# Performance work log

Hardware: AMD Instinct MI355X
Metric: run time of the kernel (lower is better)

The kernel has to match this reference:

```python
import jax, jax.numpy as jnp
import numpy as np

B, N, IN_DIM, HIDDEN, OUT_DIM, HEADS = 4, 2048, 64, 128, 128, 4
NEG_INF = -1e9
EPS = 1e-12  # matches tf.math.l2_normalize epsilon


def setup_inputs() -> dict:
    key = jax.random.key(0)
    ks = jax.random.split(key, 13)
    d1 = HIDDEN // HEADS
    d2 = OUT_DIM // HEADS
    s = lambda k, shape, fan: jax.random.normal(k, shape, jnp.float32) * (1.0 / np.sqrt(fan))
    return {
        "x": jax.random.normal(ks[0], (B, N, IN_DIM), jnp.float32),
        "embedding": s(ks[1], (N, HIDDEN), HIDDEN),
        "Wp": s(ks[2], (IN_DIM, HIDDEN), IN_DIM),
        "bp": jnp.zeros((HIDDEN,), jnp.float32),
        "W1": s(ks[3], (HIDDEN, HIDDEN), HIDDEN),
        "a1_src": s(ks[4], (HEADS, d1), d1),
        "a1_dst": s(ks[5], (HEADS, d1), d1),
        "b1": jnp.zeros((HIDDEN,), jnp.float32),
        "W2": s(ks[6], (HIDDEN, OUT_DIM), HIDDEN),
        "a2_src": s(ks[7], (HEADS, d2), d2),
        "a2_dst": s(ks[8], (HEADS, d2), d2),
        "b2": jnp.zeros((OUT_DIM,), jnp.float32),
    }


def _gat(h, mask, W, a_src, a_dst, b, heads):
    # h: [B,N,F_in], mask: [N,N] bool (adj > 0.5), W: [F_in, heads*d]
    Bn, Nn, _ = h.shape
    d = W.shape[1] // heads
    hh = (h @ W).reshape(Bn, Nn, heads, d)                 # [B,N,H,D]
    s_src = jnp.einsum('bnhd,hd->bnh', hh, a_src)          # score of source node j
    s_dst = jnp.einsum('bnhd,hd->bnh', hh, a_dst)          # score of target node i
    # e[b,i,j,h]: raw attention logit for edge j -> i
    e = jax.nn.leaky_relu(s_dst[:, :, None, :] + s_src[:, None, :, :], 0.2)
    e = jnp.where(mask[None, :, :, None], e, NEG_INF)
    alpha = jax.nn.softmax(e, axis=2)                      # softmax over neighbors j
    out = jnp.einsum('bijh,bjhd->bihd', alpha, hh)         # aggregate messages
    return out.reshape(Bn, Nn, heads * d) + b


def reference(x, embedding, Wp, bp, W1, a1_src, a1_dst, b1, W2, a2_src, a2_dst, b2):
    # AdaptiveAdjacency: cosine similarity of learned node embeddings
    ne = embedding * jax.lax.rsqrt(jnp.sum(embedding * embedding, -1, keepdims=True) + EPS)
    adj = ne @ ne.T                                        # [N,N]
    mask = adj > 0.5                                       # dynamic edge set (diag always True)
    h = x @ Wp + bp                                        # Dense projection
    h = jax.nn.gelu(_gat(h, mask, W1, a1_src, a1_dst, b1, HEADS), approximate=False)
    return _gat(h, mask, W2, a2_src, a2_dst, b2, HEADS)
```

## Files before the change

kernel.cpp:

```cpp
#include <hip/hip_runtime.h>
#include <hip/hip_bf16.h>

using u64 = unsigned long long;

constexpr int Bb    = 4;
constexpr int Nn    = 2048;
constexpr int INDIM = 64;
constexpr int HID   = 128;
constexpr int NW    = Nn / 64;
constexpr int NT    = 16;
constexpr int NTRI  = NT * (NT + 1) / 2;

struct AdjS {
    float As[32][132];
    float Bs[32][132];
    float nA[128];
    float nB[128];
    unsigned char mb [128][16];
    unsigned char mbT[128][16];
};

__global__ __launch_bounds__(256) void k_adjproj(
        const float* __restrict__ emb, u64* __restrict__ maskw,
        const float* __restrict__ x,   const float* __restrict__ Wp,
        const float* __restrict__ bp,  const float* __restrict__ W1,
        const float* __restrict__ a1s, const float* __restrict__ a1d,
        float* __restrict__ hh1, float* __restrict__ s1s, float* __restrict__ s1d) {
    __shared__ __align__(16) unsigned char smem[sizeof(AdjS)];
    const int t = threadIdx.x;

    if (blockIdx.x < NTRI) {
        AdjS& S = *reinterpret_cast<AdjS*>(smem);
        int b = blockIdx.x, ti = 0, cum = 0;
        while (cum + (NT - ti) <= b) { cum += NT - ti; ++ti; }
        const int tj = ti + (b - cum);
        const bool diag = (ti == tj);
        const int i0 = ti * 128, j0 = tj * 128;

        const int tx = t & 15, ty = t >> 4;
        const int sr = t >> 1, sh = (t & 1) * 16;

        float acc[8][8];
        #pragma unroll
        for (int a = 0; a < 8; ++a)
            #pragma unroll
            for (int c = 0; c < 8; ++c) acc[a][c] = 0.f;

        float sqa = 0.f, sqb = 0.f;

        for (int kc = 0; kc < HID; kc += 32) {
            const float* gA = emb + (size_t)(i0 + sr) * HID + kc + sh;
            const float* gB = emb + (size_t)(j0 + sr) * HID + kc + sh;
            #pragma unroll
            for (int e = 0; e < 16; e += 4) {
                const float4 va = *reinterpret_cast<const float4*>(gA + e);
                const float4 vb = *reinterpret_cast<const float4*>(gB + e);
                S.As[sh + e + 0][sr] = va.x; S.As[sh + e + 1][sr] = va.y;
                S.As[sh + e + 2][sr] = va.z; S.As[sh + e + 3][sr] = va.w;
                sqa += va.x * va.x + va.y * va.y + va.z * va.z + va.w * va.w;
                S.Bs[sh + e + 0][sr] = vb.x; S.Bs[sh + e + 1][sr] = vb.y;
                S.Bs[sh + e + 2][sr] = vb.z; S.Bs[sh + e + 3][sr] = vb.w;
                sqb += vb.x * vb.x + vb.y * vb.y + vb.z * vb.z + vb.w * vb.w;
            }
            __syncthreads();
            #pragma unroll 4
            for (int k = 0; k < 32; ++k) {
                float a[8], c[8];
                *reinterpret_cast<float4*>(&a[0]) = *reinterpret_cast<const float4*>(&S.As[k][ty * 8]);
                *reinterpret_cast<float4*>(&a[4]) = *reinterpret_cast<const float4*>(&S.As[k][ty * 8 + 4]);
                *reinterpret_cast<float4*>(&c[0]) = *reinterpret_cast<const float4*>(&S.Bs[k][tx * 8]);
                *reinterpret_cast<float4*>(&c[4]) = *reinterpret_cast<const float4*>(&S.Bs[k][tx * 8 + 4]);
                #pragma unroll
                for (int ii = 0; ii < 8; ++ii)
                    #pragma unroll
                    for (int jj = 0; jj < 8; ++jj)
                        acc[ii][jj] += a[ii] * c[jj];
            }
            __syncthreads();
        }

        {
            const float ta = sqa + __shfl_xor(sqa, 1, 64);
            if ((t & 1) == 0) S.nA[sr] = rsqrtf(ta + 1e-12f);
            const float tb = sqb + __shfl_xor(sqb, 1, 64);
            if ((t & 1) == 0) S.nB[sr] = rsqrtf(tb + 1e-12f);
        }
        __syncthreads();

        float rsi[8], rsj[8];
        #pragma unroll
        for (int e = 0; e < 8; ++e) { rsi[e] = S.nA[ty * 8 + e]; rsj[e] = S.nB[tx * 8 + e]; }

        bool bit[8][8];
        #pragma unroll
        for (int e = 0; e < 8; ++e)
            #pragma unroll
            for (int jj = 0; jj < 8; ++jj)
                bit[e][jj] = (acc[e][jj] * rsi[e] * rsj[jj] > 0.5f);

        #pragma unroll
        for (int e = 0; e < 8; ++e) {
            unsigned byte = 0;
            #pragma unroll
            for (int jj = 0; jj < 8; ++jj) if (bit[e][jj]) byte |= (1u << jj);
            S.mb[ty * 8 + e][tx] = (unsigned char)byte;
        }
        #pragma unroll
        for (int jj = 0; jj < 8; ++jj) {
            unsigned byte = 0;
            #pragma unroll
            for (int e = 0; e < 8; ++e) if (bit[e][jj]) byte |= (1u << e);
            S.mbT[tx * 8 + jj][ty] = (unsigned char)byte;
        }
        __syncthreads();

        if (t < 128) {
            const u64* p = reinterpret_cast<const u64*>(S.mb[t]);
            maskw[(size_t)(i0 + t) * NW + 2 * tj]     = p[0];
            maskw[(size_t)(i0 + t) * NW + 2 * tj + 1] = p[1];
        } else if (!diag) {
            const int c = t - 128;
            const u64* p = reinterpret_cast<const u64*>(S.mbT[c]);
            maskw[(size_t)(j0 + c) * NW + 2 * ti]     = p[0];
            maskw[(size_t)(j0 + c) * NW + 2 * ti + 1] = p[1];
        }
    } else {
        float (*hl)[128] = reinterpret_cast<float(*)[128]>(smem);
        const int h  = t >> 7;
        const int c  = t & 127;
        const int r0 = (blockIdx.x - NTRI) * 16 + h * 8;

        float acc[8];
        const float bias = bp[c];
        #pragma unroll
        for (int r = 0; r < 8; ++r) acc[r] = bias;
        #pragma unroll 4
        for (int k = 0; k < INDIM; ++k) {
            const float wp = Wp[k * HID + c];
            #pragma unroll
            for (int r = 0; r < 8; ++r)
                acc[r] += x[(size_t)(r0 + r) * INDIM + k] * wp;
        }
        #pragma unroll
        for (int r = 0; r < 8; ++r) hl[h * 8 + r][c] = acc[r];
        __syncthreads();

        float a2[8];
        #pragma unroll
        for (int r = 0; r < 8; ++r) a2[r] = 0.f;
        #pragma unroll 4
        for (int k = 0; k < HID; ++k) {
            const float w = W1[k * HID + c];
            #pragma unroll
            for (int r = 0; r < 8; ++r)
                a2[r] += hl[h * 8 + r][k] * w;
        }
        const float as = a1s[c], ad = a1d[c];
        #pragma unroll
        for (int r = 0; r < 8; ++r) {
            hh1[(size_t)(r0 + r) * HID + c] = a2[r];
            float vs = a2[r] * as;
            float vd = a2[r] * ad;
            #pragma unroll
            for (int m = 1; m < 32; m <<= 1) {
                vs += __shfl_xor(vs, m, 32);
                vd += __shfl_xor(vd, m, 32);
            }
            if ((c & 31) == 0) {
                s1s[(size_t)(r0 + r) * 4 + (c >> 5)] = vs;
                s1d[(size_t)(r0 + r) * 4 + (c >> 5)] = vd;
            }
        }
    }
}

__global__ __launch_bounds__(128) void k_layer2(
        const float* __restrict__ hh1,
        const float* __restrict__ s1s, const float* __restrict__ s1d,
        const u64* __restrict__ maskw, const float* __restrict__ b1v,
        const float* __restrict__ W2,
        const float* __restrict__ a2s, const float* __restrict__ a2d,
        const float* __restrict__ b2v, float* __restrict__ out) {
    const int r0    = blockIdx.x * 8;
    const int bb    = r0 >> 11;
    const int iBase = r0 & (Nn - 1);
    const int t     = threadIdx.x;
    const int wv    = t >> 6;
    const int lane  = t & 63;
    const int h0    = lane >> 5, h1 = 2 + h0;
    __shared__ float gl[8][128];
    __shared__ float h2l[8][128];
    __shared__ float s2sl[8][4];
    __shared__ float s2dl[8][4];

    for (int rr = 0; rr < 4; ++rr) {
        const int r   = wv * 4 + rr;
        const int row = r0 + r, i = row & (Nn - 1);
        const u64* mrow = maskw + (size_t)i * NW;
        const u64 myw = (lane < NW) ? mrow[lane] : 0ULL;
        u64 nz = __ballot(myw != 0ULL);
        const float sd0 = s1d[(size_t)row * 4 + h0];
        const float sd1 = s1d[(size_t)row * 4 + h1];
        float m0 = -INFINITY, l0 = 0.f, a0 = 0.f;
        float m1 = -INFINITY, l1 = 0.f, a1 = 0.f;
        while (nz) {
            const int w = __builtin_ctzll(nz); nz &= nz - 1;
            u64 word = __shfl(myw, w, 64);
            while (word) {
                const int bit = __builtin_ctzll(word); word &= word - 1;
                const int jr = (bb << 11) + (w << 6) + bit;
                float e0 = sd0 + s1s[(size_t)jr * 4 + h0];
                e0 = e0 > 0.f ? e0 : 0.2f * e0;
                float e1 = sd1 + s1s[(size_t)jr * 4 + h1];
                e1 = e1 > 0.f ? e1 : 0.2f * e1;
                const float v0 = hh1[(size_t)jr * HID + lane];
                const float v1 = hh1[(size_t)jr * HID + 64 + lane];
                float nm = fmaxf(m0, e0);
                float sc = __expf(m0 - nm);
                float p  = __expf(e0 - nm);
                l0 = l0 * sc + p; a0 = a0 * sc + p * v0; m0 = nm;
                nm = fmaxf(m1, e1);
                sc = __expf(m1 - nm);
                p  = __expf(e1 - nm);
                l1 = l1 * sc + p; a1 = a1 * sc + p * v1; m1 = nm;
            }
        }
        float o0 = (l0 > 0.f ? a0 / l0 : 0.f) + b1v[lane];
        float o1 = (l1 > 0.f ? a1 / l1 : 0.f) + b1v[64 + lane];
        o0 = 0.5f * o0 * (1.f + erff(o0 * 0.70710678118654752f));
        o1 = 0.5f * o1 * (1.f + erff(o1 * 0.70710678118654752f));
        gl[r][lane]      = o0;
        gl[r][64 + lane] = o1;
    }
    __syncthreads();

    {
        const int c = t;
        float acc[8];
        #pragma unroll
        for (int r = 0; r < 8; ++r) acc[r] = 0.f;
        #pragma unroll 4
        for (int k = 0; k < HID; ++k) {
            const float w = W2[k * HID + c];
            #pragma unroll
            for (int r = 0; r < 8; ++r)
                acc[r] += gl[r][k] * w;
        }
        const float as = a2s[c], ad = a2d[c];
        #pragma unroll
        for (int r = 0; r < 8; ++r) {
            h2l[r][c] = acc[r];
            float vs = acc[r] * as;
            float vd = acc[r] * ad;
            #pragma unroll
            for (int m = 1; m < 32; m <<= 1) {
                vs += __shfl_xor(vs, m, 32);
                vd += __shfl_xor(vd, m, 32);
            }
            if ((c & 31) == 0) {
                s2sl[r][c >> 5] = vs;
                s2dl[r][c >> 5] = vd;
            }
        }
    }
    __syncthreads();

    for (int rr = 0; rr < 4; ++rr) {
        const int r   = wv * 4 + rr;
        const int row = r0 + r, i = row & (Nn - 1);
        const u64* mrow = maskw + (size_t)i * NW;
        const u64 myw = (lane < NW) ? mrow[lane] : 0ULL;
        u64 nz = __ballot(myw != 0ULL);
        const float sd0 = s2dl[r][h0];
        const float sd1 = s2dl[r][h1];
        float m0 = -INFINITY, l0 = 0.f, a0 = 0.f;
        float m1 = -INFINITY, l1 = 0.f, a1 = 0.f;
        while (nz) {
            const int w = __builtin_ctzll(nz); nz &= nz - 1;
            u64 word = __shfl(myw, w, 64);
            while (word) {
                const int bit = __builtin_ctzll(word); word &= word - 1;
                const int j = (w << 6) + bit;
                float vs0, vs1, v0, v1;
                const unsigned lj = (unsigned)(j - iBase);
                if (lj < 8u) {
                    vs0 = s2sl[lj][h0]; vs1 = s2sl[lj][h1];
                    v0  = h2l[lj][lane]; v1 = h2l[lj][64 + lane];
                } else {
                    const int jr = (bb << 11) + j;
                    const u64* mrj = maskw + (size_t)j * NW;
                    const u64 myj = (lane < NW) ? mrj[lane] : 0ULL;
                    u64 nzj = __ballot(myj != 0ULL);
                    const float sdj0 = s1d[(size_t)jr * 4 + h0];
                    const float sdj1 = s1d[(size_t)jr * 4 + h1];
                    float fm0 = -INFINITY, fl0 = 0.f, fa0 = 0.f;
                    float fm1 = -INFINITY, fl1 = 0.f, fa1 = 0.f;
                    while (nzj) {
                        const int w2 = __builtin_ctzll(nzj); nzj &= nzj - 1;
                        u64 wd = __shfl(myj, w2, 64);
                        while (wd) {
                            const int b2i = __builtin_ctzll(wd); wd &= wd - 1;
                            const int k2 = (bb << 11) + (w2 << 6) + b2i;
                            float e0 = sdj0 + s1s[(size_t)k2 * 4 + h0];
                            e0 = e0 > 0.f ? e0 : 0.2f * e0;
                            float e1 = sdj1 + s1s[(size_t)k2 * 4 + h1];
                            e1 = e1 > 0.f ? e1 : 0.2f * e1;
                            const float fv0 = hh1[(size_t)k2 * HID + lane];
                            const float fv1 = hh1[(size_t)k2 * HID + 64 + lane];
                            float nm = fmaxf(fm0, e0);
                            float sc = __expf(fm0 - nm);
                            float p  = __expf(e0 - nm);
                            fl0 = fl0 * sc + p; fa0 = fa0 * sc + p * fv0; fm0 = nm;
                            nm = fmaxf(fm1, e1);
                            sc = __expf(fm1 - nm);
                            p  = __expf(e1 - nm);
                            fl1 = fl1 * sc + p; fa1 = fa1 * sc + p * fv1; fm1 = nm;
                        }
                    }
                    float g0 = (fl0 > 0.f ? fa0 / fl0 : 0.f) + b1v[lane];
                    float g1 = (fl1 > 0.f ? fa1 / fl1 : 0.f) + b1v[64 + lane];
                    g0 = 0.5f * g0 * (1.f + erff(g0 * 0.70710678118654752f));
                    g1 = 0.5f * g1 * (1.f + erff(g1 * 0.70710678118654752f));
                    float val0 = 0.f, val1 = 0.f;
                    for (int k = 0; k < 64; ++k) {
                        const float gk = __shfl(g0, k, 64);
                        val0 += gk * W2[k * HID + lane];
                        val1 += gk * W2[k * HID + 64 + lane];
                    }
                    for (int k = 0; k < 64; ++k) {
                        const float gk = __shfl(g1, k, 64);
                        val0 += gk * W2[(64 + k) * HID + lane];
                        val1 += gk * W2[(64 + k) * HID + 64 + lane];
                    }
                    float t0 = val0 * a2s[lane];
                    float t1 = val1 * a2s[64 + lane];
                    #pragma unroll
                    for (int m = 1; m < 32; m <<= 1) {
                        t0 += __shfl_xor(t0, m, 32);
                        t1 += __shfl_xor(t1, m, 32);
                    }
                    vs0 = t0; vs1 = t1; v0 = val0; v1 = val1;
                }
                float e0 = sd0 + vs0;
                e0 = e0 > 0.f ? e0 : 0.2f * e0;
                float e1 = sd1 + vs1;
                e1 = e1 > 0.f ? e1 : 0.2f * e1;
                float nm = fmaxf(m0, e0);
                float sc = __expf(m0 - nm);
                float p  = __expf(e0 - nm);
                l0 = l0 * sc + p; a0 = a0 * sc + p * v0; m0 = nm;
                nm = fmaxf(m1, e1);
                sc = __expf(m1 - nm);
                p  = __expf(e1 - nm);
                l1 = l1 * sc + p; a1 = a1 * sc + p * v1; m1 = nm;
            }
        }
        out[(size_t)row * HID + lane]      = (l0 > 0.f ? a0 / l0 : 0.f) + b2v[lane];
        out[(size_t)row * HID + 64 + lane] = (l1 > 0.f ? a1 / l1 : 0.f) + b2v[64 + lane];
    }
}

extern "C" void kernel_launch(void* const* d_in, const int* in_sizes, int n_in,
                              void* d_out, int out_size, void* d_ws, size_t ws_size,
                              hipStream_t stream) {
    const float* x   = (const float*)d_in[0];
    const float* emb = (const float*)d_in[1];
    const float* Wp  = (const float*)d_in[2];
    const float* bp  = (const float*)d_in[3];
    const float* W1  = (const float*)d_in[4];
    const float* a1s = (const float*)d_in[5];
    const float* a1d = (const float*)d_in[6];
    const float* b1  = (const float*)d_in[7];
    const float* W2  = (const float*)d_in[8];
    const float* a2s = (const float*)d_in[9];
    const float* a2d = (const float*)d_in[10];
    const float* b2  = (const float*)d_in[11];

    char* ws = (char*)d_ws;
    u64*  maskw = (u64*)ws;   ws += (size_t)Nn * NW * 8;
    float* hh1  = (float*)ws; ws += (size_t)Bb * Nn * HID * 4;
    float* s1s  = (float*)ws; ws += (size_t)Bb * Nn * 4 * 4;
    float* s1d  = (float*)ws; ws += (size_t)Bb * Nn * 4 * 4;

    k_adjproj<<<NTRI + 512, 256, 0, stream>>>(emb, maskw, x, Wp, bp, W1, a1s, a1d,
                                              hh1, s1s, s1d);
    k_layer2<<<Bb * Nn / 8, 128, 0, stream>>>(hh1, s1s, s1d, maskw, b1,
                                              W2, a2s, a2d, b2, (float*)d_out);
}
```

Baseline: 47.54 us.

## Split adjacency tiles into column halves and widen layer-2 blocks to 16 rows

Each 128x128 triangular adjacency tile is now computed by two blocks, each covering 64 columns. This doubles the number of adjacency blocks so the heavy GEMM-style phase spreads across more compute units. The mask words are packed from 4-bit nibbles, and transposed writes are restricted to 64 columns. The layer-2 kernel now processes 16 rows per block with 256 threads, so more neighbours fall inside the locally cached rows and fewer need the expensive recomputation path. The cost is fewer layer-2 blocks and more redundant A-tile loads for the adjacency phase.

```diff
diff --git a/kernel.cpp b/kernel.cpp
--- a/kernel.cpp
+++ b/kernel.cpp
@@ -10,14 +10,15 @@
 constexpr int NW    = Nn / 64;
 constexpr int NT    = 16;
 constexpr int NTRI  = NT * (NT + 1) / 2;
+constexpr int NADJ  = NTRI * 2;
 
 struct AdjS {
     float As[32][132];
-    float Bs[32][132];
+    float Bs[32][68];
     float nA[128];
-    float nB[128];
+    float nB[64];
     unsigned char mb [128][16];
-    unsigned char mbT[128][16];
+    unsigned char mbT[64][16];
 };
 
 __global__ __launch_bounds__(256) void k_adjproj(
@@ -29,51 +30,55 @@
     __shared__ __align__(16) unsigned char smem[sizeof(AdjS)];
     const int t = threadIdx.x;
 
-    if (blockIdx.x < NTRI) {
+    if (blockIdx.x < NADJ) {
         AdjS& S = *reinterpret_cast<AdjS*>(smem);
-        int b = blockIdx.x, ti = 0, cum = 0;
+        const int colHalf = blockIdx.x & 1;
+        int b = blockIdx.x >> 1, ti = 0, cum = 0;
         while (cum + (NT - ti) <= b) { cum += NT - ti; ++ti; }
         const int tj = ti + (b - cum);
         const bool diag = (ti == tj);
-        const int i0 = ti * 128, j0 = tj * 128;
+        const int i0 = ti * 128, j0 = tj * 128 + colHalf * 64;
 
         const int tx = t & 15, ty = t >> 4;
-        const int sr = t >> 1, sh = (t & 1) * 16;
-
-        float acc[8][8];
+        const int sra = t >> 1, sha = (t & 1) * 16;
+        const int srb = t >> 2, shb = (t & 3) * 8;
+
+        float acc[8][4];
         #pragma unroll
         for (int a = 0; a < 8; ++a)
             #pragma unroll
-            for (int c = 0; c < 8; ++c) acc[a][c] = 0.f;
+            for (int c = 0; c < 4; ++c) acc[a][c] = 0.f;
 
         float sqa = 0.f, sqb = 0.f;
 
         for (int kc = 0; kc < HID; kc += 32) {
-            const float* gA = emb + (size_t)(i0 + sr) * HID + kc + sh;
-            const float* gB = emb + (size_t)(j0 + sr) * HID + kc + sh;
+            const float* gA = emb + (size_t)(i0 + sra) * HID + kc + sha;
+            const float* gB = emb + (size_t)(j0 + srb) * HID + kc + shb;
             #pragma unroll
             for (int e = 0; e < 16; e += 4) {
                 const float4 va = *reinterpret_cast<const float4*>(gA + e);
+                S.As[sha + e + 0][sra] = va.x; S.As[sha + e + 1][sra] = va.y;
+                S.As[sha + e + 2][sra] = va.z; S.As[sha + e + 3][sra] = va.w;
+                sqa += va.x * va.x + va.y * va.y + va.z * va.z + va.w * va.w;
+            }
+            #pragma unroll
+            for (int e = 0; e < 8; e += 4) {
                 const float4 vb = *reinterpret_cast<const float4*>(gB + e);
-                S.As[sh + e + 0][sr] = va.x; S.As[sh + e + 1][sr] = va.y;
-                S.As[sh + e + 2][sr] = va.z; S.As[sh + e + 3][sr] = va.w;
-                sqa += va.x * va.x + va.y * va.y + va.z * va.z + va.w * va.w;
-                S.Bs[sh + e + 0][sr] = vb.x; S.Bs[sh + e + 1][sr] = vb.y;
-                S.Bs[sh + e + 2][sr] = vb.z; S.Bs[sh + e + 3][sr] = vb.w;
+                S.Bs[shb + e + 0][srb] = vb.x; S.Bs[shb + e + 1][srb] = vb.y;
+                S.Bs[shb + e + 2][srb] = vb.z; S.Bs[shb + e + 3][srb] = vb.w;
                 sqb += vb.x * vb.x + vb.y * vb.y + vb.z * vb.z + vb.w * vb.w;
             }
             __syncthreads();
             #pragma unroll 4
             for (int k = 0; k < 32; ++k) {
-                float a[8], c[8];
+                float a[8], c[4];
                 *reinterpret_cast<float4*>(&a[0]) = *reinterpret_cast<const float4*>(&S.As[k][ty * 8]);
                 *reinterpret_cast<float4*>(&a[4]) = *reinterpret_cast<const float4*>(&S.As[k][ty * 8 + 4]);
-                *reinterpret_cast<float4*>(&c[0]) = *reinterpret_cast<const float4*>(&S.Bs[k][tx * 8]);
-                *reinterpret_cast<float4*>(&c[4]) = *reinterpret_cast<const float4*>(&S.Bs[k][tx * 8 + 4]);
+                *reinterpret_cast<float4*>(&c[0]) = *reinterpret_cast<const float4*>(&S.Bs[k][tx * 4]);
                 #pragma unroll
                 for (int ii = 0; ii < 8; ++ii)
                     #pragma unroll
-                    for (int jj = 0; jj < 8; ++jj)
+                    for (int jj = 0; jj < 4; ++jj)
                         acc[ii][jj] += a[ii] * c[jj];
             }
             __syncthreads();
@@ -81,44 +86,49 @@
 
         {
             const float ta = sqa + __shfl_xor(sqa, 1, 64);
-            if ((t & 1) == 0) S.nA[sr] = rsqrtf(ta + 1e-12f);
-            const float tb = sqb + __shfl_xor(sqb, 1, 64);
-            if ((t & 1) == 0) S.nB[sr] = rsqrtf(tb + 1e-12f);
+            if ((t & 1) == 0) S.nA[sra] = rsqrtf(ta + 1e-12f);
+            float tb = sqb + __shfl_xor(sqb, 1, 64);
+            tb += __shfl_xor(tb, 2, 64);
+            if ((t & 3) == 0) S.nB[srb] = rsqrtf(tb + 1e-12f);
         }
         __syncthreads();
 
-        float rsi[8], rsj[8];
-        #pragma unroll
-        for (int e = 0; e < 8; ++e) { rsi[e] = S.nA[ty * 8 + e]; rsj[e] = S.nB[tx * 8 + e]; }
-
-        bool bit[8][8];
+        float rsi[8], rsj[4];
+        #pragma unroll
+        for (int e = 0; e < 8; ++e) rsi[e] = S.nA[ty * 8 + e];
+        #pragma unroll
+        for (int jj = 0; jj < 4; ++jj) rsj[jj] = S.nB[tx * 4 + jj];
+
+        bool bit[8][4];
         #pragma unroll
         for (int e = 0; e < 8; ++e)
             #pragma unroll
-            for (int jj = 0; jj < 8; ++jj)
+            for (int jj = 0; jj < 4; ++jj)
                 bit[e][jj] = (acc[e][jj] * rsi[e] * rsj[jj] > 0.5f);
 
         #pragma unroll
         for (int e = 0; e < 8; ++e) {
+            unsigned nib = 0;
+            #pragma unroll
+            for (int jj = 0; jj < 4; ++jj) if (bit[e][jj]) nib |= (1u << jj);
+            S.mb[ty * 8 + e][tx] = (unsigned char)nib;
+        }
+        #pragma unroll
+        for (int jj = 0; jj < 4; ++jj) {
             unsigned byte = 0;
             #pragma unroll
-            for (int jj = 0; jj < 8; ++jj) if (bit[e][jj]) byte |= (1u << jj);
-            S.mb[ty * 8 + e][tx] = (unsigned char)byte;
-        }
-        #pragma unroll
-        for (int jj = 0; jj < 8; ++jj) {
-            unsigned byte = 0;
-            #pragma unroll
             for (int e = 0; e < 8; ++e) if (bit[e][jj]) byte |= (1u << e);
-            S.mbT[tx * 8 + jj][ty] = (unsigned char)byte;
+            S.mbT[tx * 4 + jj][ty] = (unsigned char)byte;
         }
         __syncthreads();
 
         if (t < 128) {
-            const u64* p = reinterpret_cast<const u64*>(S.mb[t]);
-            maskw[(size_t)(i0 + t) * NW + 2 * tj]     = p[0];
-            maskw[(size_t)(i0 + t) * NW + 2 * tj + 1] = p[1];
-        } else if (!diag) {
+            u64 w0 = 0;
+            #pragma unroll
+            for (int n = 0; n < 16; ++n)
+                w0 |= (u64)(S.mb[t][n] & 0xF) << (4 * n);
+            maskw[(size_t)(i0 + t) * NW + 2 * tj + colHalf] = w0;
+        } else if (t < 192 && !diag) {
             const int c = t - 128;
             const u64* p = reinterpret_cast<const u64*>(S.mbT[c]);
             maskw[(size_t)(j0 + c) * NW + 2 * ti]     = p[0];
@@ -128,7 +138,7 @@
         float (*hl)[128] = reinterpret_cast<float(*)[128]>(smem);
         const int h  = t >> 7;
         const int c  = t & 127;
-        const int r0 = (blockIdx.x - NTRI) * 16 + h * 8;
+        const int r0 = (blockIdx.x - NADJ) * 16 + h * 8;
 
         float acc[8];
         const float bias = bp[c];
@@ -174,24 +184,24 @@
     }
 }
 
-__global__ __launch_bounds__(128) void k_layer2(
+__global__ __launch_bounds__(256) void k_layer2(
         const float* __restrict__ hh1,
         const float* __restrict__ s1s, const float* __restrict__ s1d,
         const u64* __restrict__ maskw, const float* __restrict__ b1v,
         const float* __restrict__ W2,
         const float* __restrict__ a2s, const float* __restrict__ a2d,
         const float* __restrict__ b2v, float* __restrict__ out) {
-    const int r0    = blockIdx.x * 8;
+    const int r0    = blockIdx.x * 16;
     const int bb    = r0 >> 11;
     const int iBase = r0 & (Nn - 1);
     const int t     = threadIdx.x;
     const int wv    = t >> 6;
     const int lane  = t & 63;
     const int h0    = lane >> 5, h1 = 2 + h0;
-    __shared__ float gl[8][128];
-    __shared__ float h2l[8][128];
-    __shared__ float s2sl[8][4];
-    __shared__ float s2dl[8][4];
+    __shared__ float gl[16][128];
+    __shared__ float h2l[16][128];
+    __shared__ float s2sl[16][4];
+    __shared__ float s2dl[16][4];
 
     for (int rr = 0; rr < 4; ++rr) {
         const int r   = wv * 4 + rr;
@@ -235,7 +245,8 @@
     __syncthreads();
 
     {
-        const int c = t;
+        const int c  = t & 127;
+        const int hf = t >> 7;
         float acc[8];
         #pragma unroll
         for (int r = 0; r < 8; ++r) acc[r] = 0.f;
@@ -244,12 +255,13 @@
             const float w = W2[k * HID + c];
             #pragma unroll
             for (int r = 0; r < 8; ++r)
-                acc[r] += gl[r][k] * w;
+                acc[r] += gl[hf * 8 + r][k] * w;
         }
         const float as = a2s[c], ad = a2d[c];
         #pragma unroll
         for (int r = 0; r < 8; ++r) {
-            h2l[r][c] = acc[r];
+            const int rr = hf * 8 + r;
+            h2l[rr][c] = acc[r];
             float vs = acc[r] * as;
             float vd = acc[r] * ad;
             #pragma unroll
@@ -258,8 +270,8 @@
                 vd += __shfl_xor(vd, m, 32);
             }
             if ((c & 31) == 0) {
-                s2sl[r][c >> 5] = vs;
-                s2dl[r][c >> 5] = vd;
+                s2sl[rr][c >> 5] = vs;
+                s2dl[rr][c >> 5] = vd;
             }
         }
     }
@@ -283,7 +295,7 @@
                 const int j = (w << 6) + bit;
                 float vs0, vs1, v0, v1;
                 const unsigned lj = (unsigned)(j - iBase);
-                if (lj < 8u) {
+                if (lj < 16u) {
                     vs0 = s2sl[lj][h0]; vs1 = s2sl[lj][h1];
                     v0  = h2l[lj][lane]; v1 = h2l[lj][64 + lane];
                 } else {
@@ -382,8 +394,8 @@
     float* s1s  = (float*)ws; ws += (size_t)Bb * Nn * 4 * 4;
     float* s1d  = (float*)ws; ws += (size_t)Bb * Nn * 4 * 4;
 
-    k_adjproj<<<NTRI + 512, 256, 0, stream>>>(emb, maskw, x, Wp, bp, W1, a1s, a1d,
+    k_adjproj<<<NADJ + 512, 256, 0, stream>>>(emb, maskw, x, Wp, bp, W1, a1s, a1d,
                                               hh1, s1s, s1d);
-    k_layer2<<<Bb * Nn / 8, 128, 0, stream>>>(hh1, s1s, s1d, maskw, b1,
-                                              W2, a2s, a2d, b2, (float*)d_out);
+    k_layer2<<<Bb * Nn / 16, 256, 0, stream>>>(hh1, s1s, s1d, maskw, b1,
+                                               W2, a2s, a2d, b2, (float*)d_out);
 }
```

Result: faster. 45.91 us (median of 2 runs) (-3.4%).
